# Kernel optimization log

Measured on AMD Instinct MI355X. Metric: run time of the kernel, lower is better.

The kernel has to match this reference:

```python
import jax, jax.numpy as jnp
import numpy as np

EPS = 1e-5  # torch BatchNorm1d default eps
HEADS = 4


def knn_idx(pcd, K):
    # pcd: (B, N, C). Torch: topk of negative squared distance -> nearest K (includes self).
    aa = jnp.sum(pcd * pcd, axis=-1)                       # (B, N)
    inner = jnp.einsum('bnc,bmc->bnm', pcd, pcd)           # (B, N, N)
    pd = 2.0 * inner - aa[:, :, None] - aa[:, None, :]     # = -||a-b||^2
    return jax.lax.top_k(pd, K)[1]                         # (B, N, K) int32


def batchnorm1d(x, gamma, beta):
    # training-mode BN over (B, C, N): stats over batch and point dims, biased var
    m = jnp.mean(x, axis=(0, 2), keepdims=True)
    v = jnp.var(x, axis=(0, 2), keepdims=True)
    return (x - m) * jax.lax.rsqrt(v + EPS) * gamma[None, :, None] + beta[None, :, None]


def setup_inputs() -> dict:
    key = jax.random.key(0)
    ks = jax.random.split(key, 8)
    B, C, N = 4, 64, 8192
    FF = 4 * C  # 256
    x = jax.random.normal(ks[0], (B, C, N), dtype=jnp.float32)
    s = 1.0 / np.sqrt(C).astype(np.float32)
    Wq = jax.random.normal(ks[1], (C, C), dtype=jnp.float32) * s
    Wk = jax.random.normal(ks[2], (C, C), dtype=jnp.float32) * s
    Wv = jax.random.normal(ks[3], (C, C), dtype=jnp.float32) * s
    W1 = jax.random.normal(ks[4], (FF, C), dtype=jnp.float32) * s
    W2 = jax.random.normal(ks[5], (C, FF), dtype=jnp.float32) * (1.0 / np.sqrt(FF).astype(np.float32))
    g1 = jnp.ones((C,), jnp.float32); b1 = jnp.zeros((C,), jnp.float32)
    g2 = jnp.ones((C,), jnp.float32); b2 = jnp.zeros((C,), jnp.float32)
    return {'x': x, 'Wq': Wq, 'Wk': Wk, 'Wv': Wv, 'W1': W1, 'W2': W2,
            'g1': g1, 'b1': b1, 'g2': g2, 'b2': b2, 'K': 40}


def reference(x, Wq, Wk, Wv, W1, W2, g1, b1, g2, b2, K):
    B, C, N = x.shape
    H = HEADS
    D = C // H
    pcd = jnp.transpose(x, (0, 2, 1))                      # (B, N, C)
    idx = knn_idx(pcd, K)                                  # (B, N, K)
    nbr = jax.vmap(lambda p, i: p[i])(pcd, idx)            # (B, N, K, C) gather
    diff = nbr - pcd[:, :, None, :]                        # group_type='diff'
    # 1x1 conv projections
    q = jnp.einsum('oc,bnc->bno', Wq, pcd)                 # (B, N, C)
    k = jnp.einsum('oc,bnkc->bnko', Wk, diff)              # (B, N, K, C)
    v = jnp.einsum('oc,bnkc->bnko', Wv, diff)
    # split heads: channel = (H D), H-major
    qh = q.reshape(B, N, H, D)
    kh = k.reshape(B, N, K, H, D)
    vh = v.reshape(B, N, K, H, D)
    scale = np.float32(np.sqrt(D))
    energy = jnp.einsum('bnhd,bnkhd->bnhk', qh, kh) / scale
    attn = jax.nn.softmax(energy, axis=-1)
    out = jnp.einsum('bnhk,bnkhd->bnhd', attn, vh)         # (B, N, H, D)
    tmp = jnp.transpose(out.reshape(B, N, C), (0, 2, 1))   # (B, C, N)
    x1 = batchnorm1d(x + tmp, g1, b1)
    h = jax.nn.leaky_relu(jnp.einsum('oc,bcn->bon', W1, x1), 0.2)
    ff = jnp.einsum('co,bon->bcn', W2, h)
    return batchnorm1d(x1 + ff, g2, b2)
```

## Files before the change

### kernel.cpp

```cpp
#include <hip/hip_runtime.h>

#define Bc 4
#define Cc 64
#define Nc 8192
#define Kc 40
#define CN (Cc * Nc)

__global__ __launch_bounds__(256) void aa_kernel(const float* __restrict__ x,
                                                 float* __restrict__ aa) {
  const int e = blockIdx.x * 256 + threadIdx.x;
  const int b = e >> 13, n = e & 8191;
  const float* xb = x + (size_t)b * CN + n;
  float s = 0.f;
#pragma unroll
  for (int c = 0; c < 64; ++c) {
    const float v = xb[c * Nc];
    s = fmaf(v, v, s);
  }
  aa[e] = s;
}

__global__ __launch_bounds__(256) void proj_kernel(
    const float* __restrict__ x, const float* __restrict__ Wq,
    const float* __restrict__ Wk, const float* __restrict__ Wv,
    float* __restrict__ qp, float* __restrict__ kp, float* __restrict__ vp) {
  __shared__ float xs[64 * 64];
  __shared__ float wt[64 * 64];
  const int t = threadIdx.x;
  const int w = t >> 6, lane = t & 63;
  const int b = blockIdx.x >> 7;
  const int n0 = (blockIdx.x & 127) << 6;
  const float* xb = x + (size_t)b * CN;
  for (int c = w; c < 64; c += 4) xs[c * 64 + lane] = xb[c * Nc + n0 + lane];

  const float* Ws[3] = {Wq, Wk, Wv};
  float* Ds[3] = {qp, kp, vp};
  for (int mtx = 0; mtx < 3; ++mtx) {
    __syncthreads();
    const float* W = Ws[mtx];
    for (int q = t; q < 4096; q += 256) {
      const int o = q & 63, c = q >> 6;
      wt[c * 64 + o] = W[o * 64 + c];
    }
    __syncthreads();
    float acc[16];
#pragma unroll
    for (int k = 0; k < 16; ++k) acc[k] = 0.f;
#pragma unroll 8
    for (int c = 0; c < 64; ++c) {
      const float xv = xs[c * 64 + lane];
      const float4 w0 = *(const float4*)&wt[c * 64 + w * 16 + 0];
      const float4 w1 = *(const float4*)&wt[c * 64 + w * 16 + 4];
      const float4 w2 = *(const float4*)&wt[c * 64 + w * 16 + 8];
      const float4 w3 = *(const float4*)&wt[c * 64 + w * 16 + 12];
      acc[0] = fmaf(xv, w0.x, acc[0]);   acc[1] = fmaf(xv, w0.y, acc[1]);
      acc[2] = fmaf(xv, w0.z, acc[2]);   acc[3] = fmaf(xv, w0.w, acc[3]);
      acc[4] = fmaf(xv, w1.x, acc[4]);   acc[5] = fmaf(xv, w1.y, acc[5]);
      acc[6] = fmaf(xv, w1.z, acc[6]);   acc[7] = fmaf(xv, w1.w, acc[7]);
      acc[8] = fmaf(xv, w2.x, acc[8]);   acc[9] = fmaf(xv, w2.y, acc[9]);
      acc[10] = fmaf(xv, w2.z, acc[10]); acc[11] = fmaf(xv, w2.w, acc[11]);
      acc[12] = fmaf(xv, w3.x, acc[12]); acc[13] = fmaf(xv, w3.y, acc[13]);
      acc[14] = fmaf(xv, w3.z, acc[14]); acc[15] = fmaf(xv, w3.w, acc[15]);
    }
    float* dst = Ds[mtx] + ((size_t)(b * Nc + n0 + lane)) * 64 + w * 16;
    *(float4*)(dst + 0) = make_float4(acc[0], acc[1], acc[2], acc[3]);
    *(float4*)(dst + 4) = make_float4(acc[4], acc[5], acc[6], acc[7]);
    *(float4*)(dst + 8) = make_float4(acc[8], acc[9], acc[10], acc[11]);
    *(float4*)(dst + 12) = make_float4(acc[12], acc[13], acc[14], acc[15]);
  }
}

__global__ __launch_bounds__(256) void knn_kernel(const float* __restrict__ x,
                                                  const float* __restrict__ aa,
                                                  int* __restrict__ knn) {
  __shared__ float rowT[64 * 64];
  __shared__ float colT[64 * 64];
  __shared__ float qv[64 * 64];
  __shared__ unsigned short qidx[64 * 64];
  __shared__ int qcnt[64];
  __shared__ float thr[64];

  const int t = threadIdx.x;
  const int w = t >> 6;
  const int lane = t & 63;
  const int b = blockIdx.x >> 7;
  const int i0 = (blockIdx.x & 127) << 6;
  const float* xb = x + (size_t)b * CN;
  const float* aab = aa + b * Nc;

  for (int c = w; c < 64; c += 4) rowT[c * 64 + lane] = xb[c * Nc + i0 + lane];
  if (t < 64) { qcnt[t] = 0; thr[t] = -INFINITY; }

  const int tr = t >> 4;
  const int tc = t & 15;
  const float4 rA4 = *(const float4*)&aab[i0 + tr * 4];
  const float rA[4] = {rA4.x, rA4.y, rA4.z, rA4.w};

  float lv[40]; int li[40];
#pragma unroll
  for (int q2 = 0; q2 < 40; ++q2) { lv[q2] = -INFINITY; li[q2] = 0; }
  float lmin = -INFINITY; int lminpos = 0;

  __syncthreads();

  for (int jt = 0; jt < 128; ++jt) {
    const int j0 = jt << 6;

    if (w == 0) {
      const int r = lane;
      const int cnt = qcnt[r];
      for (int e2 = 0; e2 < cnt; ++e2) {
        const float v = qv[r * 64 + e2];
        if (v > lmin) {
          const int jj = (int)qidx[r * 64 + e2];
#pragma unroll
          for (int q2 = 0; q2 < 40; ++q2)
            if (q2 == lminpos) { lv[q2] = v; li[q2] = jj; }
          float nm = lv[0]; int np2 = 0;
#pragma unroll
          for (int q2 = 1; q2 < 40; ++q2) {
            const bool lt = lv[q2] < nm;
            nm = lt ? lv[q2] : nm;
            np2 = lt ? q2 : np2;
          }
          lmin = nm; lminpos = np2;
        }
      }
      qcnt[r] = 0;
      thr[r] = lmin;
    }
    for (int c = w; c < 64; c += 4) colT[c * 64 + lane] = xb[c * Nc + j0 + lane];
    __syncthreads();

    float acc[4][4];
#pragma unroll
    for (int i = 0; i < 4; ++i)
#pragma unroll
      for (int jj = 0; jj < 4; ++jj) acc[i][jj] = 0.f;

#pragma unroll 16
    for (int c = 0; c < 64; ++c) {
      const float4 av = *(const float4*)&rowT[c * 64 + tr * 4];
      const float4 bv = *(const float4*)&colT[c * 64 + tc * 4];
      acc[0][0] = fmaf(av.x, bv.x, acc[0][0]); acc[0][1] = fmaf(av.x, bv.y, acc[0][1]);
      acc[0][2] = fmaf(av.x, bv.z, acc[0][2]); acc[0][3] = fmaf(av.x, bv.w, acc[0][3]);
      acc[1][0] = fmaf(av.y, bv.x, acc[1][0]); acc[1][1] = fmaf(av.y, bv.y, acc[1][1]);
      acc[1][2] = fmaf(av.y, bv.z, acc[1][2]); acc[1][3] = fmaf(av.y, bv.w, acc[1][3]);
      acc[2][0] = fmaf(av.z, bv.x, acc[2][0]); acc[2][1] = fmaf(av.z, bv.y, acc[2][1]);
      acc[2][2] = fmaf(av.z, bv.z, acc[2][2]); acc[2][3] = fmaf(av.z, bv.w, acc[2][3]);
      acc[3][0] = fmaf(av.w, bv.x, acc[3][0]); acc[3][1] = fmaf(av.w, bv.y, acc[3][1]);
      acc[3][2] = fmaf(av.w, bv.z, acc[3][2]); acc[3][3] = fmaf(av.w, bv.w, acc[3][3]);
    }

    const float4 cA4 = *(const float4*)&aab[j0 + tc * 4];
    const float cA[4] = {cA4.x, cA4.y, cA4.z, cA4.w};
#pragma unroll
    for (int i = 0; i < 4; ++i) {
      const int r = tr * 4 + i;
      const float th = thr[r];
#pragma unroll
      for (int jj = 0; jj < 4; ++jj) {
        const float v = 2.0f * acc[i][jj] - rA[i] - cA[jj];
        if (v > th) {
          const int pos = atomicAdd(&qcnt[r], 1);
          qv[r * 64 + pos] = v;
          qidx[r * 64 + pos] = (unsigned short)(j0 + tc * 4 + jj);
        }
      }
    }
    __syncthreads();
  }

  if (w == 0) {
    const int r = lane;
    const int cnt = qcnt[r];
    for (int e2 = 0; e2 < cnt; ++e2) {
      const float v = qv[r * 64 + e2];
      if (v > lmin) {
        const int jj = (int)qidx[r * 64 + e2];
#pragma unroll
        for (int q2 = 0; q2 < 40; ++q2)
          if (q2 == lminpos) { lv[q2] = v; li[q2] = jj; }
        float nm = lv[0]; int np2 = 0;
#pragma unroll
        for (int q2 = 1; q2 < 40; ++q2) {
          const bool lt = lv[q2] < nm;
          nm = lt ? lv[q2] : nm;
          np2 = lt ? q2 : np2;
        }
        lmin = nm; lminpos = np2;
      }
    }
    int* dst = knn + (size_t)(b * Nc + i0 + r) * Kc;
#pragma unroll
    for (int q2 = 0; q2 < 40; ++q2) dst[q2] = li[q2];
  }
}

__global__ __launch_bounds__(256) void attn_kernel(
    const float* __restrict__ x, const float* __restrict__ qp,
    const float* __restrict__ kp, const float* __restrict__ vp,
    const int* __restrict__ knn, float* __restrict__ y) {
  const int lane = threadIdx.x & 63;
  const int wid = threadIdx.x >> 6;
  const int pt = (blockIdx.x << 2) + wid;
  const int b = pt >> 13;
  const int nn = pt & 8191;
  const float q = qp[(size_t)pt * 64 + lane];
  const float vself = vp[(size_t)pt * 64 + lane];
  const float* kpb = kp + (size_t)b * (Nc * 64);
  const float* vpb = vp + (size_t)b * (Nc * 64);
  const int* idn = knn + (size_t)pt * Kc;
  float e[40], vv[40];
#pragma unroll
  for (int j = 0; j < 40; ++j) {
    const int ij = idn[j];
    const float kj = kpb[ij * 64 + lane];
    vv[j] = vpb[ij * 64 + lane];
    float p = q * kj;
    p += __shfl_xor(p, 1);
    p += __shfl_xor(p, 2);
    p += __shfl_xor(p, 4);
    p += __shfl_xor(p, 8);
    e[j] = p * 0.25f;
  }
  float m = e[0];
#pragma unroll
  for (int j = 1; j < 40; ++j) m = fmaxf(m, e[j]);
  float s = 0.f;
#pragma unroll
  for (int j = 0; j < 40; ++j) { e[j] = __expf(e[j] - m); s += e[j]; }
  const float inv = 1.f / s;
  float acc = 0.f;
#pragma unroll
  for (int j = 0; j < 40; ++j) acc = fmaf(e[j] * inv, vv[j], acc);
  const size_t xi = (size_t)b * CN + (size_t)lane * Nc + nn;
  y[xi] = x[xi] + (acc - vself);
}

__global__ __launch_bounds__(256) void stats_kernel(const float* __restrict__ src,
                                                    float* __restrict__ out) {
  const int c = blockIdx.x;
  float s = 0.f, s2 = 0.f;
  for (int b = 0; b < Bc; ++b) {
    const float* p = src + (size_t)b * CN + (size_t)c * Nc;
    for (int i = threadIdx.x; i < Nc; i += 256) {
      const float v = p[i];
      s += v;
      s2 = fmaf(v, v, s2);
    }
  }
  __shared__ float rs[256], rs2[256];
  rs[threadIdx.x] = s; rs2[threadIdx.x] = s2;
  __syncthreads();
  for (int st = 128; st > 0; st >>= 1) {
    if (threadIdx.x < st) {
      rs[threadIdx.x] += rs[threadIdx.x + st];
      rs2[threadIdx.x] += rs2[threadIdx.x + st];
    }
    __syncthreads();
  }
  if (threadIdx.x == 0) {
    const float mean = rs[0] * (1.f / 32768.f);
    const float var = rs2[0] * (1.f / 32768.f) - mean * mean;
    out[c] = mean;
    out[64 + c] = 1.f / sqrtf(var + 1e-5f);
  }
}

__global__ __launch_bounds__(256) void w2t_kernel(const float* __restrict__ W2,
                                                  float* __restrict__ W2t) {
  const int e = blockIdx.x * 256 + threadIdx.x;
  const int o = e >> 6, c = e & 63;
  W2t[e] = W2[c * 256 + o];
}

__global__ __launch_bounds__(256) void ffn_kernel(
    const float* __restrict__ y, const float* __restrict__ W1,
    const float* __restrict__ W2t, const float* __restrict__ st1,
    const float* __restrict__ g1, const float* __restrict__ b1,
    float* __restrict__ z) {
  const int pt = blockIdx.x * 256 + threadIdx.x;
  const int b = pt >> 13, nn = pt & 8191;
  const float* yb = y + (size_t)b * CN + nn;
  float x1[64], z0[64];
#pragma unroll
  for (int c = 0; c < 64; ++c) {
    const float sc = st1[64 + c] * g1[c];
    x1[c] = (yb[(size_t)c * Nc] - st1[c]) * sc + b1[c];
    z0[c] = x1[c];
  }
  for (int o = 0; o < 256; ++o) {
    const float* w1r = W1 + o * 64;
    float hv = 0.f;
#pragma unroll
    for (int c = 0; c < 64; ++c) hv = fmaf(w1r[c], x1[c], hv);
    hv = hv >= 0.f ? hv : 0.2f * hv;
    const float* w2r = W2t + o * 64;
#pragma unroll
    for (int c = 0; c < 64; ++c) z0[c] = fmaf(w2r[c], hv, z0[c]);
  }
  float* zb = z + (size_t)b * CN + nn;
#pragma unroll
  for (int c = 0; c < 64; ++c) zb[(size_t)c * Nc] = z0[c];
}

__global__ __launch_bounds__(256) void bn_apply_kernel(
    const float* __restrict__ z, const float* __restrict__ st2,
    const float* __restrict__ g2, const float* __restrict__ b2,
    float* __restrict__ out) {
  const int e = blockIdx.x * 256 + threadIdx.x;
  const int c = (e >> 13) & 63;
  const float sc = st2[64 + c] * g2[c];
  out[e] = (z[e] - st2[c]) * sc + b2[c];
}

extern "C" void kernel_launch(void* const* d_in, const int* in_sizes, int n_in,
                              void* d_out, int out_size, void* d_ws, size_t ws_size,
                              hipStream_t stream) {
  (void)in_sizes; (void)n_in; (void)out_size; (void)ws_size;
  const float* x  = (const float*)d_in[0];
  const float* Wq = (const float*)d_in[1];
  const float* Wk = (const float*)d_in[2];
  const float* Wv = (const float*)d_in[3];
  const float* W1 = (const float*)d_in[4];
  const float* W2 = (const float*)d_in[5];
  const float* g1 = (const float*)d_in[6];
  const float* b1 = (const float*)d_in[7];
  const float* g2 = (const float*)d_in[8];
  const float* b2 = (const float*)d_in[9];
  float* out = (float*)d_out;

  float* ws = (float*)d_ws;
  float* aa  = ws;
  float* qp  = aa + 32768;
  float* kp  = qp + 2097152;
  float* vp  = kp + 2097152;
  float* y   = vp + 2097152;
  float* z   = y + 2097152;
  float* st1 = z + 2097152;
  float* st2 = st1 + 128;
  float* W2t = st2 + 128;
  int* knn   = (int*)(W2t + 16384);

  hipLaunchKernelGGL(aa_kernel, dim3(128), dim3(256), 0, stream, x, aa);
  hipLaunchKernelGGL(proj_kernel, dim3(512), dim3(256), 0, stream, x, Wq, Wk, Wv, qp, kp, vp);
  hipLaunchKernelGGL(knn_kernel, dim3(512), dim3(256), 0, stream, x, aa, knn);
  hipLaunchKernelGGL(attn_kernel, dim3(8192), dim3(256), 0, stream, x, qp, kp, vp, knn, y);
  hipLaunchKernelGGL(stats_kernel, dim3(64), dim3(256), 0, stream, y, st1);
  hipLaunchKernelGGL(w2t_kernel, dim3(64), dim3(256), 0, stream, W2, W2t);
  hipLaunchKernelGGL(ffn_kernel, dim3(128), dim3(256), 0, stream, y, W1, W2t, st1, g1, b1, z);
  hipLaunchKernelGGL(stats_kernel, dim3(64), dim3(256), 0, stream, z, st2);
  hipLaunchKernelGGL(bn_apply_kernel, dim3(8192), dim3(256), 0, stream, z, st2, g2, b2, out);
}
```

Before: 1.639 ms.

## Enlarge kNN tiles to 128x128 and split top-k merging across all threads

The kNN kernel now computes 128x128 distance tiles with an 8x8 register block per thread, raising arithmetic reuse per shared-memory load. The candidate queues are drained twice per tile by all 256 threads, two per row, each keeping a partial top-40 list. The two partial lists are merged at the end. Before, a single wave did all the insertion work, which serialised it. The grid is halved to 256 blocks with one block per CU, so latency hiding now depends on the larger per-thread work and the higher register pressure.

```diff
diff --git a/kernel.cpp b/kernel.cpp
--- a/kernel.cpp
+++ b/kernel.cpp
@@ -70,130 +70,160 @@
   }
 }
 
-__global__ __launch_bounds__(256) void knn_kernel(const float* __restrict__ x,
-                                                  const float* __restrict__ aa,
-                                                  int* __restrict__ knn) {
-  __shared__ float rowT[64 * 64];
-  __shared__ float colT[64 * 64];
-  __shared__ float qv[64 * 64];
-  __shared__ unsigned short qidx[64 * 64];
-  __shared__ int qcnt[64];
-  __shared__ float thr[64];
+__global__ __launch_bounds__(256, 1) void knn_kernel(const float* __restrict__ x,
+                                                     const float* __restrict__ aa,
+                                                     int* __restrict__ knn) {
+  __shared__ float rowT[64][128];
+  __shared__ float colT[64][128];
+  __shared__ float qv[128][64];
+  __shared__ unsigned short qidx[128][64];
+  __shared__ float thrS[128][2];
+  __shared__ int qcnt[128];
 
   const int t = threadIdx.x;
-  const int w = t >> 6;
-  const int lane = t & 63;
-  const int b = blockIdx.x >> 7;
-  const int i0 = (blockIdx.x & 127) << 6;
+  const int ty = t >> 4;
+  const int tx = t & 15;
+  const int b = blockIdx.x >> 6;
+  const int i0 = (blockIdx.x & 63) << 7;
   const float* xb = x + (size_t)b * CN;
   const float* aab = aa + b * Nc;
 
-  for (int c = w; c < 64; c += 4) rowT[c * 64 + lane] = xb[c * Nc + i0 + lane];
-  if (t < 64) { qcnt[t] = 0; thr[t] = -INFINITY; }
-
-  const int tr = t >> 4;
-  const int tc = t & 15;
-  const float4 rA4 = *(const float4*)&aab[i0 + tr * 4];
-  const float rA[4] = {rA4.x, rA4.y, rA4.z, rA4.w};
+  if (t < 128) { qcnt[t] = 0; thrS[t][0] = -INFINITY; thrS[t][1] = -INFINITY; }
+
+  const int cSub = t >> 4;
+  const int chunk = t & 15;
+  for (int cc = 0; cc < 4; ++cc) {
+    const int c = cc * 16 + cSub;
+    const float* src = xb + (size_t)c * Nc + i0 + chunk * 8;
+    const float4 v0 = ((const float4*)src)[0];
+    const float4 v1 = ((const float4*)src)[1];
+    *(float4*)&rowT[c][chunk * 8] = v0;
+    *(float4*)&rowT[c][chunk * 8 + 4] = v1;
+  }
+
+  float rA[8];
+  {
+    const float4 r0 = *(const float4*)&aab[i0 + ty * 8];
+    const float4 r1 = *(const float4*)&aab[i0 + ty * 8 + 4];
+    rA[0] = r0.x; rA[1] = r0.y; rA[2] = r0.z; rA[3] = r0.w;
+    rA[4] = r1.x; rA[5] = r1.y; rA[6] = r1.z; rA[7] = r1.w;
+  }
 
   float lv[40]; int li[40];
 #pragma unroll
-  for (int q2 = 0; q2 < 40; ++q2) { lv[q2] = -INFINITY; li[q2] = 0; }
+  for (int q = 0; q < 40; ++q) { lv[q] = -INFINITY; li[q] = 0; }
   float lmin = -INFINITY; int lminpos = 0;
 
-  __syncthreads();
-
-  for (int jt = 0; jt < 128; ++jt) {
-    const int j0 = jt << 6;
-
-    if (w == 0) {
-      const int r = lane;
-      const int cnt = qcnt[r];
-      for (int e2 = 0; e2 < cnt; ++e2) {
-        const float v = qv[r * 64 + e2];
-        if (v > lmin) {
-          const int jj = (int)qidx[r * 64 + e2];
-#pragma unroll
-          for (int q2 = 0; q2 < 40; ++q2)
-            if (q2 == lminpos) { lv[q2] = v; li[q2] = jj; }
-          float nm = lv[0]; int np2 = 0;
-#pragma unroll
-          for (int q2 = 1; q2 < 40; ++q2) {
-            const bool lt = lv[q2] < nm;
-            nm = lt ? lv[q2] : nm;
-            np2 = lt ? q2 : np2;
+  const int dr = t >> 1, slot = t & 1;
+
+  auto insert = [&](float v, int idx) {
+#pragma unroll
+    for (int q = 0; q < 40; ++q)
+      if (q == lminpos) { lv[q] = v; li[q] = idx; }
+    float nm = lv[0]; int np = 0;
+#pragma unroll
+    for (int q = 1; q < 40; ++q) {
+      if (lv[q] < nm) { nm = lv[q]; np = q; }
+    }
+    lmin = nm; lminpos = np;
+  };
+
+  for (int jt = 0; jt < 64; ++jt) {
+    const int j0 = jt << 7;
+    for (int cc = 0; cc < 4; ++cc) {
+      const int c = cc * 16 + cSub;
+      const float* src = xb + (size_t)c * Nc + j0 + chunk * 8;
+      const float4 v0 = ((const float4*)src)[0];
+      const float4 v1 = ((const float4*)src)[1];
+      *(float4*)&colT[c][chunk * 8] = v0;
+      *(float4*)&colT[c][chunk * 8 + 4] = v1;
+    }
+    __syncthreads();
+
+    float acc[8][8];
+#pragma unroll
+    for (int i = 0; i < 8; ++i)
+#pragma unroll
+      for (int jj = 0; jj < 8; ++jj) acc[i][jj] = 0.f;
+
+#pragma unroll 2
+    for (int c = 0; c < 64; ++c) {
+      const float4 a0 = *(const float4*)&rowT[c][ty * 8];
+      const float4 a1 = *(const float4*)&rowT[c][ty * 8 + 4];
+      const float4 b0 = *(const float4*)&colT[c][tx * 4];
+      const float4 b1 = *(const float4*)&colT[c][64 + tx * 4];
+      const float av[8] = {a0.x, a0.y, a0.z, a0.w, a1.x, a1.y, a1.z, a1.w};
+      const float bv[8] = {b0.x, b0.y, b0.z, b0.w, b1.x, b1.y, b1.z, b1.w};
+#pragma unroll
+      for (int i = 0; i < 8; ++i)
+#pragma unroll
+        for (int jj = 0; jj < 8; ++jj)
+          acc[i][jj] = fmaf(av[i], bv[jj], acc[i][jj]);
+    }
+
+    float cA[8];
+    {
+      const float4 c0 = *(const float4*)&aab[j0 + tx * 4];
+      const float4 c1 = *(const float4*)&aab[j0 + 64 + tx * 4];
+      cA[0] = c0.x; cA[1] = c0.y; cA[2] = c0.z; cA[3] = c0.w;
+      cA[4] = c1.x; cA[5] = c1.y; cA[6] = c1.z; cA[7] = c1.w;
+    }
+
+    for (int half = 0; half < 2; ++half) {
+      float th8[8];
+      {
+        const float4* tp = (const float4*)&thrS[ty * 8][0];
+        const float4 u0 = tp[0], u1 = tp[1], u2 = tp[2], u3 = tp[3];
+        th8[0] = fminf(u0.x, u0.y); th8[1] = fminf(u0.z, u0.w);
+        th8[2] = fminf(u1.x, u1.y); th8[3] = fminf(u1.z, u1.w);
+        th8[4] = fminf(u2.x, u2.y); th8[5] = fminf(u2.z, u2.w);
+        th8[6] = fminf(u3.x, u3.y); th8[7] = fminf(u3.z, u3.w);
+      }
+#pragma unroll
+      for (int i = 0; i < 8; ++i) {
+        const int r = ty * 8 + i;
+#pragma unroll
+        for (int jq = 0; jq < 4; ++jq) {
+          const int jj = half * 4 + jq;
+          const float v = 2.0f * acc[i][jj] - rA[i] - cA[jj];
+          if (v > th8[i]) {
+            const int pos = atomicAdd(&qcnt[r], 1);
+            qv[r][pos] = v;
+            qidx[r][pos] = (unsigned short)(j0 + half * 64 + tx * 4 + jq);
           }
-          lmin = nm; lminpos = np2;
         }
       }
-      qcnt[r] = 0;
-      thr[r] = lmin;
-    }
-    for (int c = w; c < 64; c += 4) colT[c * 64 + lane] = xb[c * Nc + j0 + lane];
-    __syncthreads();
-
-    float acc[4][4];
-#pragma unroll
-    for (int i = 0; i < 4; ++i)
-#pragma unroll
-      for (int jj = 0; jj < 4; ++jj) acc[i][jj] = 0.f;
-
-#pragma unroll 16
-    for (int c = 0; c < 64; ++c) {
-      const float4 av = *(const float4*)&rowT[c * 64 + tr * 4];
-      const float4 bv = *(const float4*)&colT[c * 64 + tc * 4];
-      acc[0][0] = fmaf(av.x, bv.x, acc[0][0]); acc[0][1] = fmaf(av.x, bv.y, acc[0][1]);
-      acc[0][2] = fmaf(av.x, bv.z, acc[0][2]); acc[0][3] = fmaf(av.x, bv.w, acc[0][3]);
-      acc[1][0] = fmaf(av.y, bv.x, acc[1][0]); acc[1][1] = fmaf(av.y, bv.y, acc[1][1]);
-      acc[1][2] = fmaf(av.y, bv.z, acc[1][2]); acc[1][3] = fmaf(av.y, bv.w, acc[1][3]);
-      acc[2][0] = fmaf(av.z, bv.x, acc[2][0]); acc[2][1] = fmaf(av.z, bv.y, acc[2][1]);
-      acc[2][2] = fmaf(av.z, bv.z, acc[2][2]); acc[2][3] = fmaf(av.z, bv.w, acc[2][3]);
-      acc[3][0] = fmaf(av.w, bv.x, acc[3][0]); acc[3][1] = fmaf(av.w, bv.y, acc[3][1]);
-      acc[3][2] = fmaf(av.w, bv.z, acc[3][2]); acc[3][3] = fmaf(av.w, bv.w, acc[3][3]);
-    }
-
-    const float4 cA4 = *(const float4*)&aab[j0 + tc * 4];
-    const float cA[4] = {cA4.x, cA4.y, cA4.z, cA4.w};
-#pragma unroll
-    for (int i = 0; i < 4; ++i) {
-      const int r = tr * 4 + i;
-      const float th = thr[r];
-#pragma unroll
-      for (int jj = 0; jj < 4; ++jj) {
-        const float v = 2.0f * acc[i][jj] - rA[i] - cA[jj];
-        if (v > th) {
-          const int pos = atomicAdd(&qcnt[r], 1);
-          qv[r * 64 + pos] = v;
-          qidx[r * 64 + pos] = (unsigned short)(j0 + tc * 4 + jj);
+      __syncthreads();
+      {
+        int cnt = qcnt[dr]; if (cnt > 64) cnt = 64;
+        for (int e = slot; e < cnt; e += 2) {
+          const float v = qv[dr][e];
+          if (v > lmin) insert(v, (int)qidx[dr][e]);
         }
+        if (slot == 0) qcnt[dr] = 0;
+        thrS[dr][slot] = lmin;
       }
-    }
-    __syncthreads();
-  }
-
-  if (w == 0) {
-    const int r = lane;
-    const int cnt = qcnt[r];
-    for (int e2 = 0; e2 < cnt; ++e2) {
-      const float v = qv[r * 64 + e2];
-      if (v > lmin) {
-        const int jj = (int)qidx[r * 64 + e2];
-#pragma unroll
-        for (int q2 = 0; q2 < 40; ++q2)
-          if (q2 == lminpos) { lv[q2] = v; li[q2] = jj; }
-        float nm = lv[0]; int np2 = 0;
-#pragma unroll
-        for (int q2 = 1; q2 < 40; ++q2) {
-          const bool lt = lv[q2] < nm;
-          nm = lt ? lv[q2] : nm;
-          np2 = lt ? q2 : np2;
-        }
-        lmin = nm; lminpos = np2;
-      }
-    }
-    int* dst = knn + (size_t)(b * Nc + i0 + r) * Kc;
-#pragma unroll
-    for (int q2 = 0; q2 < 40; ++q2) dst[q2] = li[q2];
+      __syncthreads();
+    }
+  }
+
+  if (slot == 1) {
+#pragma unroll
+    for (int q = 0; q < 40; ++q) {
+      qv[dr][q] = lv[q];
+      qidx[dr][q] = (unsigned short)li[q];
+    }
+  }
+  __syncthreads();
+  if (slot == 0) {
+#pragma unroll
+    for (int q = 0; q < 40; ++q) {
+      const float v = qv[dr][q];
+      if (v > lmin) insert(v, (int)qidx[dr][q]);
+    }
+    int* dst = knn + (size_t)(b * Nc + i0 + dr) * Kc;
+#pragma unroll
+    for (int q = 0; q < 40; ++q) dst[q] = li[q];
   }
 }
 
@@ -345,7 +375,7 @@
 
   hipLaunchKernelGGL(aa_kernel, dim3(128), dim3(256), 0, stream, x, aa);
   hipLaunchKernelGGL(proj_kernel, dim3(512), dim3(256), 0, stream, x, Wq, Wk, Wv, qp, kp, vp);
-  hipLaunchKernelGGL(knn_kernel, dim3(512), dim3(256), 0, stream, x, aa, knn);
+  hipLaunchKernelGGL(knn_kernel, dim3(256), dim3(256), 0, stream, x, aa, knn);
   hipLaunchKernelGGL(attn_kernel, dim3(8192), dim3(256), 0, stream, x, qp, kp, vp, knn, y);
   hipLaunchKernelGGL(stats_kernel, dim3(64), dim3(256), 0, stream, y, st1);
   hipLaunchKernelGGL(w2t_kernel, dim3(64), dim3(256), 0, stream, W2, W2t);
```

Result: slower. 1.840 ms (+12.3%).
